# Performance work log

Measured on AMD Instinct MI355X. Metric: run time of the kernel, lower is better.

The kernel has to match this reference:

```python
import jax, jax.numpy as jnp
import numpy as np

B = 1048576
EPS = 1e-5

def _lin_params(key, din, dout):
    k1, k2 = jax.random.split(key)
    bound = 1.0 / np.sqrt(din)
    w = jax.random.uniform(k1, (din, dout), minval=-bound, maxval=bound, dtype=jnp.float32)
    b = jax.random.uniform(k2, (dout,), minval=-bound, maxval=bound, dtype=jnp.float32)
    return w, b

def setup_inputs() -> dict:
    key = jax.random.key(0)
    ks = jax.random.split(key, 10)
    x = jax.random.normal(ks[0], (B, 8), dtype=jnp.float32)
    dims = [(8, 16), (16, 16), (16, 12), (12, 8), (8, 4), (4, 4), (4, 4), (4, 1)]
    names = ['fm', 'c1', 'p1', 'c2', 'p2', 'c3', 'r', 'h']
    inp = {'x': x,
           'bn_g': jnp.ones((8,), jnp.float32),
           'bn_b': jnp.zeros((8,), jnp.float32)}
    for i, (nm, (di, do)) in enumerate(zip(names, dims)):
        w, b = _lin_params(ks[i + 1], di, do)
        inp['w_' + nm] = w
        inp['b_' + nm] = b
    return inp

def reference(x, bn_g, bn_b, w_fm, b_fm, w_c1, b_c1, w_p1, b_p1, w_c2, b_c2,
              w_p2, b_p2, w_c3, b_c3, w_r, b_r, w_h, b_h):
    # BatchNorm1d (training mode): batch statistics, biased variance
    mu = jnp.mean(x, axis=0)
    var = jnp.mean((x - mu) ** 2, axis=0)
    h = (x - mu) * jax.lax.rsqrt(var + EPS) * bn_g + bn_b
    h = jnp.tanh(h @ w_fm + b_fm)   # [B,16] feature_map
    h = jnp.tanh(h @ w_c1 + b_c1)   # [B,16] conv1
    h = jnp.tanh(h @ w_p1 + b_p1)   # [B,12] pool1
    h = jnp.tanh(h @ w_c2 + b_c2)   # [B,8]  conv2
    h = jnp.tanh(h @ w_p2 + b_p2)   # [B,4]  pool2
    h = jnp.tanh(h @ w_c3 + b_c3)   # [B,4]  conv3
    res = jax.nn.relu(h @ w_r + b_r)  # [B,4] residual branch
    h = h + res
    return jax.nn.sigmoid(h @ w_h + b_h)  # [B,1]
```

## Files before the change

### kernel.cpp

```cpp
#include <hip/hip_runtime.h>
#include <stdint.h>

#define B_ROWS 1048576
#define STAT_BLOCKS 512
#define MAIN_BLOCKS 2048

typedef __fp16 h2 __attribute__((ext_vector_type(2)));

#define PART_OFF 16
#define WPK_OFF 8208
#define BIA_OFF 8578
#define W_FM 0
#define W_C1 64
#define W_P1 192
#define W_C2 288
#define W_P2 336
#define W_C3 352
#define W_R  360
#define W_H  368
#define B_FM 0
#define B_C1 16
#define B_P1 32
#define B_C2 44
#define B_P2 52
#define B_C3 56
#define B_R  60
#define B_H  64

__device__ __forceinline__ float exp_tanh(float x) {
    float e = __builtin_amdgcn_exp2f(x * 2.8853900817779268f);
    return 1.0f - 2.0f * __builtin_amdgcn_rcpf(e + 1.0f);
}

__device__ __forceinline__ float fast_sigmoid(float x) {
    float e = __builtin_amdgcn_exp2f(x * -1.4426950408889634f);
    return __builtin_amdgcn_rcpf(1.0f + e);
}

template<int DIN, int DOUT>
__device__ void pack_layer(const float* __restrict__ w, const float* __restrict__ b,
                           uint32_t* __restrict__ wdst, float* __restrict__ bdst) {
    for (int idx = threadIdx.x; idx < DOUT * (DIN / 2); idx += blockDim.x) {
        int j = idx / (DIN / 2), i2 = idx % (DIN / 2);
        h2 h;
        h.x = (__fp16)w[(2 * i2) * DOUT + j];
        h.y = (__fp16)w[(2 * i2 + 1) * DOUT + j];
        wdst[j * (DIN / 2) + i2] = __builtin_bit_cast(uint32_t, h);
    }
    for (int j = threadIdx.x; j < DOUT; j += blockDim.x) bdst[j] = b[j];
}

__global__ __launch_bounds__(256) void bn_stats(
    const float* __restrict__ x, float* __restrict__ ws,
    const float* __restrict__ w_fm, const float* __restrict__ b_fm,
    const float* __restrict__ w_c1, const float* __restrict__ b_c1,
    const float* __restrict__ w_p1, const float* __restrict__ b_p1,
    const float* __restrict__ w_c2, const float* __restrict__ b_c2,
    const float* __restrict__ w_p2, const float* __restrict__ b_p2,
    const float* __restrict__ w_c3, const float* __restrict__ b_c3,
    const float* __restrict__ w_r,  const float* __restrict__ b_r,
    const float* __restrict__ w_h,  const float* __restrict__ b_h)
{
    const int tid = blockIdx.x * 256 + threadIdx.x;
    float s[8], q[8];
#pragma unroll
    for (int c = 0; c < 8; ++c) { s[c] = 0.f; q[c] = 0.f; }
    const float4* x4 = (const float4*)x;
#pragma unroll
    for (int k = 0; k < 8; ++k) {
        int r = tid + k * 131072;
        float4 a = x4[2 * r];
        float4 b = x4[2 * r + 1];
        s[0] += a.x; s[1] += a.y; s[2] += a.z; s[3] += a.w;
        s[4] += b.x; s[5] += b.y; s[6] += b.z; s[7] += b.w;
        q[0] += a.x * a.x; q[1] += a.y * a.y; q[2] += a.z * a.z; q[3] += a.w * a.w;
        q[4] += b.x * b.x; q[5] += b.y * b.y; q[6] += b.z * b.z; q[7] += b.w * b.w;
    }
#pragma unroll
    for (int off = 32; off > 0; off >>= 1) {
#pragma unroll
        for (int c = 0; c < 8; ++c) {
            s[c] += __shfl_down(s[c], off);
            q[c] += __shfl_down(q[c], off);
        }
    }
    __shared__ float red[4][16];
    const int lane = threadIdx.x & 63;
    const int wave = threadIdx.x >> 6;
    if (lane == 0) {
#pragma unroll
        for (int c = 0; c < 8; ++c) { red[wave][c] = s[c]; red[wave][8 + c] = q[c]; }
    }
    __syncthreads();
    if (threadIdx.x < 16) {
        float acc = red[0][threadIdx.x] + red[1][threadIdx.x] +
                    red[2][threadIdx.x] + red[3][threadIdx.x];
        ws[PART_OFF + blockIdx.x * 16 + threadIdx.x] = acc;
    }
    if (blockIdx.x == 0) {
        uint32_t* wpk = (uint32_t*)(ws + WPK_OFF);
        float*    bpk = ws + BIA_OFF;
        pack_layer<8, 16>(w_fm, b_fm, wpk + W_FM, bpk + B_FM);
        pack_layer<16,16>(w_c1, b_c1, wpk + W_C1, bpk + B_C1);
        pack_layer<16,12>(w_p1, b_p1, wpk + W_P1, bpk + B_P1);
        pack_layer<12, 8>(w_c2, b_c2, wpk + W_C2, bpk + B_C2);
        pack_layer<8,  4>(w_p2, b_p2, wpk + W_P2, bpk + B_P2);
        pack_layer<4,  4>(w_c3, b_c3, wpk + W_C3, bpk + B_C3);
        pack_layer<4,  4>(w_r,  b_r,  wpk + W_R,  bpk + B_R);
        pack_layer<4,  1>(w_h,  b_h,  wpk + W_H,  bpk + B_H);
    }
}

__device__ __forceinline__ float lut_tanh(float x, const float* __restrict__ lut) {
    float t = fmaf(x, 1024.0f, 4096.0f);
    t = __builtin_amdgcn_fmed3f(t, 0.0f, 8191.0f);
    return lut[(int)t];
}

template<int DIN, int DOUT>
__device__ __forceinline__ void layer_dot(const h2* __restrict__ apkA, const h2* __restrict__ apkB,
                                          float* __restrict__ outA, float* __restrict__ outB,
                                          const uint32_t* __restrict__ wpk,
                                          const float* __restrict__ bias) {
#pragma unroll
    for (int j = 0; j < DOUT; ++j) {
        float accA = bias[j];
        float accB = accA;
#pragma unroll
        for (int i2 = 0; i2 < DIN / 2; ++i2) {
            h2 w = __builtin_bit_cast(h2, wpk[j * (DIN / 2) + i2]);
            accA = __builtin_amdgcn_fdot2(apkA[i2], w, accA, false);
            accB = __builtin_amdgcn_fdot2(apkB[i2], w, accB, false);
        }
        outA[j] = accA;
        outB[j] = accB;
    }
}

template<int N>
__device__ __forceinline__ void tanh_pack(const float* __restrict__ inA, const float* __restrict__ inB,
                                          h2* __restrict__ pkA, h2* __restrict__ pkB,
                                          const float* __restrict__ lut) {
#pragma unroll
    for (int k = 0; k < N / 2; ++k) {
        float a0 = lut_tanh(inA[2 * k], lut);
        float a1 = lut_tanh(inA[2 * k + 1], lut);
        float b0 = lut_tanh(inB[2 * k], lut);
        float b1 = lut_tanh(inB[2 * k + 1], lut);
        pkA[k] = __builtin_amdgcn_cvt_pkrtz(a0, a1);
        pkB[k] = __builtin_amdgcn_cvt_pkrtz(b0, b1);
    }
}

__global__ __launch_bounds__(256) void qcnn_main(
    const float* __restrict__ x,
    const float* __restrict__ bn_g, const float* __restrict__ bn_b,
    const float* __restrict__ ws, float* __restrict__ out)
{
    const int tid = blockIdx.x * 256 + threadIdx.x;
    const int r0 = tid, r1 = tid + (B_ROWS / 2);
    const float4* x4 = (const float4*)x;
    float4 xa0 = x4[2 * r0], xa1 = x4[2 * r0 + 1];
    float4 xb0 = x4[2 * r1], xb1 = x4[2 * r1 + 1];

    __shared__ float lut[8192];
    __shared__ float accs[16][17];
    __shared__ float scs[8], shs[8];

    {
        const float h = 0.0009765625f;
#pragma unroll
        for (int k = 0; k < 32; ++k) {
            int i = threadIdx.x + k * 256;
            float xc = fmaf((float)i + 0.5f, h, -4.0f);
            lut[i] = exp_tanh(xc);
        }
    }
    {
        const int f = threadIdx.x & 15;
        const int chunk = threadIdx.x >> 4;
        const float* p = ws + PART_OFF + (chunk * 32) * 16 + f;
        float a = 0.f;
#pragma unroll 8
        for (int b = 0; b < 32; ++b) a += p[b * 16];
        accs[chunk][f] = a;
    }
    __syncthreads();
    if (threadIdx.x < 16) {
        float t = 0.f;
#pragma unroll
        for (int c = 0; c < 16; ++c) t += accs[c][threadIdx.x];
        accs[0][threadIdx.x] = t;
    }
    __syncthreads();
    if (threadIdx.x < 8) {
        const float invB = 1.0f / (float)B_ROWS;
        int c = threadIdx.x;
        float mu  = accs[0][c] * invB;
        float var = fmaf(-mu, mu, accs[0][8 + c] * invB);
        float s   = bn_g[c] * rsqrtf(var + 1e-5f);
        scs[c] = s;
        shs[c] = fmaf(-mu, s, bn_b[c]);
    }
    __syncthreads();

    float sc[8], sh[8];
#pragma unroll
    for (int c = 0; c < 8; ++c) { sc[c] = scs[c]; sh[c] = shs[c]; }

    const uint32_t* wpk = (const uint32_t*)(ws + WPK_OFF);
    const float*    bpk = ws + BIA_OFF;

    float nA[8], nB[8];
    nA[0] = fmaf(xa0.x, sc[0], sh[0]); nA[1] = fmaf(xa0.y, sc[1], sh[1]);
    nA[2] = fmaf(xa0.z, sc[2], sh[2]); nA[3] = fmaf(xa0.w, sc[3], sh[3]);
    nA[4] = fmaf(xa1.x, sc[4], sh[4]); nA[5] = fmaf(xa1.y, sc[5], sh[5]);
    nA[6] = fmaf(xa1.z, sc[6], sh[6]); nA[7] = fmaf(xa1.w, sc[7], sh[7]);
    nB[0] = fmaf(xb0.x, sc[0], sh[0]); nB[1] = fmaf(xb0.y, sc[1], sh[1]);
    nB[2] = fmaf(xb0.z, sc[2], sh[2]); nB[3] = fmaf(xb0.w, sc[3], sh[3]);
    nB[4] = fmaf(xb1.x, sc[4], sh[4]); nB[5] = fmaf(xb1.y, sc[5], sh[5]);
    nB[6] = fmaf(xb1.z, sc[6], sh[6]); nB[7] = fmaf(xb1.w, sc[7], sh[7]);
    h2 a8[4], b8[4];
#pragma unroll
    for (int k = 0; k < 4; ++k) {
        a8[k] = __builtin_amdgcn_cvt_pkrtz(nA[2 * k], nA[2 * k + 1]);
        b8[k] = __builtin_amdgcn_cvt_pkrtz(nB[2 * k], nB[2 * k + 1]);
    }

    float oA[16], oB[16]; h2 pA[8], pB[8];
    layer_dot<8, 16>(a8, b8, oA, oB, wpk + W_FM, bpk + B_FM);
    tanh_pack<16>(oA, oB, pA, pB, lut);
    float o2A[16], o2B[16]; h2 p2A[8], p2B[8];
    layer_dot<16,16>(pA, pB, o2A, o2B, wpk + W_C1, bpk + B_C1);
    tanh_pack<16>(o2A, o2B, p2A, p2B, lut);
    float o3A[12], o3B[12]; h2 p3A[6], p3B[6];
    layer_dot<16,12>(p2A, p2B, o3A, o3B, wpk + W_P1, bpk + B_P1);
    tanh_pack<12>(o3A, o3B, p3A, p3B, lut);
    float o4A[8], o4B[8]; h2 p4A[4], p4B[4];
    layer_dot<12, 8>(p3A, p3B, o4A, o4B, wpk + W_C2, bpk + B_C2);
    tanh_pack<8>(o4A, o4B, p4A, p4B, lut);
    float o5A[4], o5B[4]; h2 p5A[2], p5B[2];
    layer_dot<8,  4>(p4A, p4B, o5A, o5B, wpk + W_P2, bpk + B_P2);
    tanh_pack<4>(o5A, o5B, p5A, p5B, lut);
    float c4A[4], c4B[4];
    layer_dot<4,  4>(p5A, p5B, c4A, c4B, wpk + W_C3, bpk + B_C3);
#pragma unroll
    for (int j = 0; j < 4; ++j) {
        c4A[j] = lut_tanh(c4A[j], lut);
        c4B[j] = lut_tanh(c4B[j], lut);
    }
    h2 pcA[2], pcB[2];
    pcA[0] = __builtin_amdgcn_cvt_pkrtz(c4A[0], c4A[1]);
    pcA[1] = __builtin_amdgcn_cvt_pkrtz(c4A[2], c4A[3]);
    pcB[0] = __builtin_amdgcn_cvt_pkrtz(c4B[0], c4B[1]);
    pcB[1] = __builtin_amdgcn_cvt_pkrtz(c4B[2], c4B[3]);
    float r4A[4], r4B[4];
    layer_dot<4,  4>(pcA, pcB, r4A, r4B, wpk + W_R, bpk + B_R);
#pragma unroll
    for (int j = 0; j < 4; ++j) {
        c4A[j] += fmaxf(r4A[j], 0.f);
        c4B[j] += fmaxf(r4B[j], 0.f);
    }
    h2 phA[2], phB[2];
    phA[0] = __builtin_amdgcn_cvt_pkrtz(c4A[0], c4A[1]);
    phA[1] = __builtin_amdgcn_cvt_pkrtz(c4A[2], c4A[3]);
    phB[0] = __builtin_amdgcn_cvt_pkrtz(c4B[0], c4B[1]);
    phB[1] = __builtin_amdgcn_cvt_pkrtz(c4B[2], c4B[3]);
    float ohA[1], ohB[1];
    layer_dot<4,  1>(phA, phB, ohA, ohB, wpk + W_H, bpk + B_H);
    out[r0] = fast_sigmoid(ohA[0]);
    out[r1] = fast_sigmoid(ohB[0]);
}

extern "C" void kernel_launch(void* const* d_in, const int* in_sizes, int n_in,
                              void* d_out, int out_size, void* d_ws, size_t ws_size,
                              hipStream_t stream) {
    const float* x    = (const float*)d_in[0];
    const float* bn_g = (const float*)d_in[1];
    const float* bn_b = (const float*)d_in[2];
    const float* w_fm = (const float*)d_in[3];
    const float* b_fm = (const float*)d_in[4];
    const float* w_c1 = (const float*)d_in[5];
    const float* b_c1 = (const float*)d_in[6];
    const float* w_p1 = (const float*)d_in[7];
    const float* b_p1 = (const float*)d_in[8];
    const float* w_c2 = (const float*)d_in[9];
    const float* b_c2 = (const float*)d_in[10];
    const float* w_p2 = (const float*)d_in[11];
    const float* b_p2 = (const float*)d_in[12];
    const float* w_c3 = (const float*)d_in[13];
    const float* b_c3 = (const float*)d_in[14];
    const float* w_r  = (const float*)d_in[15];
    const float* b_r  = (const float*)d_in[16];
    const float* w_h  = (const float*)d_in[17];
    const float* b_h  = (const float*)d_in[18];
    float* out = (float*)d_out;
    float* ws  = (float*)d_ws;

    bn_stats<<<STAT_BLOCKS, 256, 0, stream>>>(
        x, ws, w_fm, b_fm, w_c1, b_c1, w_p1, b_p1, w_c2, b_c2,
        w_p2, b_p2, w_c3, b_c3, w_r, b_r, w_h, b_h);
    qcnn_main<<<MAIN_BLOCKS, 256, 0, stream>>>(x, bn_g, bn_b, ws, out);
}
```

Measured before the change: 142.0 us.

## Split BN finalize into own kernel, use fp16 tanh LUT, process rows sequentially

The batch-statistics finalize step moves out of every main block into a separate single-block kernel that writes scale and shift into the workspace. The tanh lookup table shrinks from fp32 to fp16, halving its LDS footprint and letting packed fp16 activations be built directly from the table entries. Each thread now runs its two rows one after the other instead of interleaved, and launch bounds request 6 blocks per CU. Together these aim to cut register and LDS pressure and per-block setup to raise occupancy, at the cost of an extra kernel launch and less ILP per thread.

```diff
diff --git a/kernel.cpp b/kernel.cpp
--- a/kernel.cpp
+++ b/kernel.cpp
@@ -111,51 +111,128 @@
     }
 }
 
-__device__ __forceinline__ float lut_tanh(float x, const float* __restrict__ lut) {
+__global__ __launch_bounds__(256) void bn_finalize(
+    const float* __restrict__ bn_g, const float* __restrict__ bn_b,
+    float* __restrict__ ws)
+{
+    __shared__ float accs[16][17];
+    const int f = threadIdx.x & 15;
+    const int chunk = threadIdx.x >> 4;
+    const float* p = ws + PART_OFF + (chunk * 32) * 16 + f;
+    float a = 0.f;
+#pragma unroll 8
+    for (int b = 0; b < 32; ++b) a += p[b * 16];
+    accs[chunk][f] = a;
+    __syncthreads();
+    if (threadIdx.x < 16) {
+        float t = 0.f;
+#pragma unroll
+        for (int c = 0; c < 16; ++c) t += accs[c][threadIdx.x];
+        accs[0][threadIdx.x] = t;
+    }
+    __syncthreads();
+    if (threadIdx.x < 8) {
+        const float invB = 1.0f / (float)B_ROWS;
+        int c = threadIdx.x;
+        float mu  = accs[0][c] * invB;
+        float var = fmaf(-mu, mu, accs[0][8 + c] * invB);
+        float sv  = bn_g[c] * rsqrtf(var + 1e-5f);
+        ws[c]     = sv;
+        ws[8 + c] = fmaf(-mu, sv, bn_b[c]);
+    }
+}
+
+__device__ __forceinline__ uint32_t lut_idx(float x) {
     float t = fmaf(x, 1024.0f, 4096.0f);
     t = __builtin_amdgcn_fmed3f(t, 0.0f, 8191.0f);
-    return lut[(int)t];
+    return (uint32_t)t;
 }
 
 template<int DIN, int DOUT>
-__device__ __forceinline__ void layer_dot(const h2* __restrict__ apkA, const h2* __restrict__ apkB,
-                                          float* __restrict__ outA, float* __restrict__ outB,
-                                          const uint32_t* __restrict__ wpk,
-                                          const float* __restrict__ bias) {
+__device__ __forceinline__ void layer_dot1(const h2* __restrict__ apk,
+                                           float* __restrict__ o,
+                                           const uint32_t* __restrict__ wpk,
+                                           const float* __restrict__ bias) {
 #pragma unroll
     for (int j = 0; j < DOUT; ++j) {
-        float accA = bias[j];
-        float accB = accA;
+        float acc = bias[j];
 #pragma unroll
         for (int i2 = 0; i2 < DIN / 2; ++i2) {
             h2 w = __builtin_bit_cast(h2, wpk[j * (DIN / 2) + i2]);
-            accA = __builtin_amdgcn_fdot2(apkA[i2], w, accA, false);
-            accB = __builtin_amdgcn_fdot2(apkB[i2], w, accB, false);
+            acc = __builtin_amdgcn_fdot2(apk[i2], w, acc, false);
         }
-        outA[j] = accA;
-        outB[j] = accB;
+        o[j] = acc;
     }
 }
 
 template<int N>
-__device__ __forceinline__ void tanh_pack(const float* __restrict__ inA, const float* __restrict__ inB,
-                                          h2* __restrict__ pkA, h2* __restrict__ pkB,
-                                          const float* __restrict__ lut) {
+__device__ __forceinline__ void tanh_pack1(const float* __restrict__ in,
+                                           h2* __restrict__ pk,
+                                           const uint16_t* __restrict__ lut16) {
 #pragma unroll
     for (int k = 0; k < N / 2; ++k) {
-        float a0 = lut_tanh(inA[2 * k], lut);
-        float a1 = lut_tanh(inA[2 * k + 1], lut);
-        float b0 = lut_tanh(inB[2 * k], lut);
-        float b1 = lut_tanh(inB[2 * k + 1], lut);
-        pkA[k] = __builtin_amdgcn_cvt_pkrtz(a0, a1);
-        pkB[k] = __builtin_amdgcn_cvt_pkrtz(b0, b1);
-    }
-}
-
-__global__ __launch_bounds__(256) void qcnn_main(
-    const float* __restrict__ x,
-    const float* __restrict__ bn_g, const float* __restrict__ bn_b,
-    const float* __restrict__ ws, float* __restrict__ out)
+        uint32_t v0 = lut16[lut_idx(in[2 * k])];
+        uint32_t v1 = lut16[lut_idx(in[2 * k + 1])];
+        pk[k] = __builtin_bit_cast(h2, v0 | (v1 << 16));
+    }
+}
+
+__device__ __forceinline__ float row_forward(float4 x0, float4 x1,
+        const float* __restrict__ sc, const float* __restrict__ sh,
+        const uint32_t* __restrict__ wpk, const float* __restrict__ bpk,
+        const uint16_t* __restrict__ lut16) {
+    float n[8];
+    n[0] = fmaf(x0.x, sc[0], sh[0]); n[1] = fmaf(x0.y, sc[1], sh[1]);
+    n[2] = fmaf(x0.z, sc[2], sh[2]); n[3] = fmaf(x0.w, sc[3], sh[3]);
+    n[4] = fmaf(x1.x, sc[4], sh[4]); n[5] = fmaf(x1.y, sc[5], sh[5]);
+    n[6] = fmaf(x1.z, sc[6], sh[6]); n[7] = fmaf(x1.w, sc[7], sh[7]);
+    h2 a[4];
+#pragma unroll
+    for (int k = 0; k < 4; ++k)
+        a[k] = __builtin_amdgcn_cvt_pkrtz(n[2 * k], n[2 * k + 1]);
+
+    float o1[16]; h2 p1[8];
+    layer_dot1<8, 16>(a, o1, wpk + W_FM, bpk + B_FM);
+    tanh_pack1<16>(o1, p1, lut16);
+    float o2[16]; h2 p2[8];
+    layer_dot1<16,16>(p1, o2, wpk + W_C1, bpk + B_C1);
+    tanh_pack1<16>(o2, p2, lut16);
+    float o3[12]; h2 p3[6];
+    layer_dot1<16,12>(p2, o3, wpk + W_P1, bpk + B_P1);
+    tanh_pack1<12>(o3, p3, lut16);
+    float o4[8]; h2 p4[4];
+    layer_dot1<12, 8>(p3, o4, wpk + W_C2, bpk + B_C2);
+    tanh_pack1<8>(o4, p4, lut16);
+    float o5[4]; h2 p5[2];
+    layer_dot1<8,  4>(p4, o5, wpk + W_P2, bpk + B_P2);
+    tanh_pack1<4>(o5, p5, lut16);
+    float c4[4];
+    layer_dot1<4,  4>(p5, c4, wpk + W_C3, bpk + B_C3);
+
+    uint32_t u[4]; float f[4];
+#pragma unroll
+    for (int j = 0; j < 4; ++j) {
+        u[j] = lut16[lut_idx(c4[j])];
+        f[j] = (float)__builtin_bit_cast(__fp16, (uint16_t)u[j]);
+    }
+    h2 pc[2];
+    pc[0] = __builtin_bit_cast(h2, u[0] | (u[1] << 16));
+    pc[1] = __builtin_bit_cast(h2, u[2] | (u[3] << 16));
+    float r4[4];
+    layer_dot1<4,  4>(pc, r4, wpk + W_R, bpk + B_R);
+#pragma unroll
+    for (int j = 0; j < 4; ++j) f[j] += fmaxf(r4[j], 0.f);
+    h2 ph[2];
+    ph[0] = __builtin_amdgcn_cvt_pkrtz(f[0], f[1]);
+    ph[1] = __builtin_amdgcn_cvt_pkrtz(f[2], f[3]);
+    float oh[1];
+    layer_dot1<4,  1>(ph, oh, wpk + W_H, bpk + B_H);
+    return fast_sigmoid(oh[0]);
+}
+
+__global__ __launch_bounds__(256, 6) void qcnn_main(
+    const float* __restrict__ x, const float* __restrict__ ws,
+    float* __restrict__ out)
 {
     const int tid = blockIdx.x * 256 + threadIdx.x;
     const int r0 = tid, r1 = tid + (B_ROWS / 2);
@@ -163,113 +240,31 @@
     float4 xa0 = x4[2 * r0], xa1 = x4[2 * r0 + 1];
     float4 xb0 = x4[2 * r1], xb1 = x4[2 * r1 + 1];
 
-    __shared__ float lut[8192];
-    __shared__ float accs[16][17];
-    __shared__ float scs[8], shs[8];
-
+    __shared__ uint16_t lut16[8192];
     {
         const float h = 0.0009765625f;
-#pragma unroll
-        for (int k = 0; k < 32; ++k) {
-            int i = threadIdx.x + k * 256;
-            float xc = fmaf((float)i + 0.5f, h, -4.0f);
-            lut[i] = exp_tanh(xc);
+        uint32_t* l32 = (uint32_t*)lut16;
+#pragma unroll
+        for (int k = 0; k < 16; ++k) {
+            int i2 = threadIdx.x + k * 256;
+            float c0 = fmaf((float)(2 * i2) + 0.5f, h, -4.0f);
+            float c1 = fmaf((float)(2 * i2 + 1) + 0.5f, h, -4.0f);
+            __fp16 h0 = (__fp16)exp_tanh(c0);
+            __fp16 h1 = (__fp16)exp_tanh(c1);
+            l32[i2] = (uint32_t)__builtin_bit_cast(uint16_t, h0)
+                    | ((uint32_t)__builtin_bit_cast(uint16_t, h1) << 16);
         }
     }
-    {
-        const int f = threadIdx.x & 15;
-        const int chunk = threadIdx.x >> 4;
-        const float* p = ws + PART_OFF + (chunk * 32) * 16 + f;
-        float a = 0.f;
-#pragma unroll 8
-        for (int b = 0; b < 32; ++b) a += p[b * 16];
-        accs[chunk][f] = a;
-    }
+    float sc[8], sh[8];
+#pragma unroll
+    for (int c = 0; c < 8; ++c) { sc[c] = ws[c]; sh[c] = ws[8 + c]; }
     __syncthreads();
-    if (threadIdx.x < 16) {
-        float t = 0.f;
-#pragma unroll
-        for (int c = 0; c < 16; ++c) t += accs[c][threadIdx.x];
-        accs[0][threadIdx.x] = t;
-    }
-    __syncthreads();
-    if (threadIdx.x < 8) {
-        const float invB = 1.0f / (float)B_ROWS;
-        int c = threadIdx.x;
-        float mu  = accs[0][c] * invB;
-        float var = fmaf(-mu, mu, accs[0][8 + c] * invB);
-        float s   = bn_g[c] * rsqrtf(var + 1e-5f);
-        scs[c] = s;
-        shs[c] = fmaf(-mu, s, bn_b[c]);
-    }
-    __syncthreads();
-
-    float sc[8], sh[8];
-#pragma unroll
-    for (int c = 0; c < 8; ++c) { sc[c] = scs[c]; sh[c] = shs[c]; }
 
     const uint32_t* wpk = (const uint32_t*)(ws + WPK_OFF);
     const float*    bpk = ws + BIA_OFF;
 
-    float nA[8], nB[8];
-    nA[0] = fmaf(xa0.x, sc[0], sh[0]); nA[1] = fmaf(xa0.y, sc[1], sh[1]);
-    nA[2] = fmaf(xa0.z, sc[2], sh[2]); nA[3] = fmaf(xa0.w, sc[3], sh[3]);
-    nA[4] = fmaf(xa1.x, sc[4], sh[4]); nA[5] = fmaf(xa1.y, sc[5], sh[5]);
-    nA[6] = fmaf(xa1.z, sc[6], sh[6]); nA[7] = fmaf(xa1.w, sc[7], sh[7]);
-    nB[0] = fmaf(xb0.x, sc[0], sh[0]); nB[1] = fmaf(xb0.y, sc[1], sh[1]);
-    nB[2] = fmaf(xb0.z, sc[2], sh[2]); nB[3] = fmaf(xb0.w, sc[3], sh[3]);
-    nB[4] = fmaf(xb1.x, sc[4], sh[4]); nB[5] = fmaf(xb1.y, sc[5], sh[5]);
-    nB[6] = fmaf(xb1.z, sc[6], sh[6]); nB[7] = fmaf(xb1.w, sc[7], sh[7]);
-    h2 a8[4], b8[4];
-#pragma unroll
-    for (int k = 0; k < 4; ++k) {
-        a8[k] = __builtin_amdgcn_cvt_pkrtz(nA[2 * k], nA[2 * k + 1]);
-        b8[k] = __builtin_amdgcn_cvt_pkrtz(nB[2 * k], nB[2 * k + 1]);
-    }
-
-    float oA[16], oB[16]; h2 pA[8], pB[8];
-    layer_dot<8, 16>(a8, b8, oA, oB, wpk + W_FM, bpk + B_FM);
-    tanh_pack<16>(oA, oB, pA, pB, lut);
-    float o2A[16], o2B[16]; h2 p2A[8], p2B[8];
-    layer_dot<16,16>(pA, pB, o2A, o2B, wpk + W_C1, bpk + B_C1);
-    tanh_pack<16>(o2A, o2B, p2A, p2B, lut);
-    float o3A[12], o3B[12]; h2 p3A[6], p3B[6];
-    layer_dot<16,12>(p2A, p2B, o3A, o3B, wpk + W_P1, bpk + B_P1);
-    tanh_pack<12>(o3A, o3B, p3A, p3B, lut);
-    float o4A[8], o4B[8]; h2 p4A[4], p4B[4];
-    layer_dot<12, 8>(p3A, p3B, o4A, o4B, wpk + W_C2, bpk + B_C2);
-    tanh_pack<8>(o4A, o4B, p4A, p4B, lut);
-    float o5A[4], o5B[4]; h2 p5A[2], p5B[2];
-    layer_dot<8,  4>(p4A, p4B, o5A, o5B, wpk + W_P2, bpk + B_P2);
-    tanh_pack<4>(o5A, o5B, p5A, p5B, lut);
-    float c4A[4], c4B[4];
-    layer_dot<4,  4>(p5A, p5B, c4A, c4B, wpk + W_C3, bpk + B_C3);
-#pragma unroll
-    for (int j = 0; j < 4; ++j) {
-        c4A[j] = lut_tanh(c4A[j], lut);
-        c4B[j] = lut_tanh(c4B[j], lut);
-    }
-    h2 pcA[2], pcB[2];
-    pcA[0] = __builtin_amdgcn_cvt_pkrtz(c4A[0], c4A[1]);
-    pcA[1] = __builtin_amdgcn_cvt_pkrtz(c4A[2], c4A[3]);
-    pcB[0] = __builtin_amdgcn_cvt_pkrtz(c4B[0], c4B[1]);
-    pcB[1] = __builtin_amdgcn_cvt_pkrtz(c4B[2], c4B[3]);
-    float r4A[4], r4B[4];
-    layer_dot<4,  4>(pcA, pcB, r4A, r4B, wpk + W_R, bpk + B_R);
-#pragma unroll
-    for (int j = 0; j < 4; ++j) {
-        c4A[j] += fmaxf(r4A[j], 0.f);
-        c4B[j] += fmaxf(r4B[j], 0.f);
-    }
-    h2 phA[2], phB[2];
-    phA[0] = __builtin_amdgcn_cvt_pkrtz(c4A[0], c4A[1]);
-    phA[1] = __builtin_amdgcn_cvt_pkrtz(c4A[2], c4A[3]);
-    phB[0] = __builtin_amdgcn_cvt_pkrtz(c4B[0], c4B[1]);
-    phB[1] = __builtin_amdgcn_cvt_pkrtz(c4B[2], c4B[3]);
-    float ohA[1], ohB[1];
-    layer_dot<4,  1>(phA, phB, ohA, ohB, wpk + W_H, bpk + B_H);
-    out[r0] = fast_sigmoid(ohA[0]);
-    out[r1] = fast_sigmoid(ohB[0]);
+    out[r0] = row_forward(xa0, xa1, sc, sh, wpk, bpk, lut16);
+    out[r1] = row_forward(xb0, xb1, sc, sh, wpk, bpk, lut16);
 }
 
 extern "C" void kernel_launch(void* const* d_in, const int* in_sizes, int n_in,
@@ -300,5 +295,6 @@
     bn_stats<<<STAT_BLOCKS, 256, 0, stream>>>(
         x, ws, w_fm, b_fm, w_c1, b_c1, w_p1, b_p1, w_c2, b_c2,
         w_p2, b_p2, w_c3, b_c3, w_r, b_r, w_h, b_h);
-    qcnn_main<<<MAIN_BLOCKS, 256, 0, stream>>>(x, bn_g, bn_b, ws, out);
-}
+    bn_finalize<<<1, 256, 0, stream>>>(bn_g, bn_b, ws);
+    qcnn_main<<<MAIN_BLOCKS, 256, 0, stream>>>(x, ws, out);
+}
```

Result: no change. 141.0 us (-0.7%).

## Replace shared-memory tanh LUT with direct exp-based tanh and adjacent-row pairing

Applied to the files above, without the earlier changes.

Removes the 32KB per-block shared tanh lookup table and its per-block construction, computing tanh directly through exp_tanh in registers. This removes the LUT build cost in every block and the LDS footprint that limited occupancy, and launch bounds now request 4 blocks per SIMD. Each thread now processes two adjacent rows, so x loads are contiguous 64-byte reads and the outputs go out as one float2 store. The tradeoff is more ALU work per activation, since each tanh now needs an exp and a divide instead of a table load, plus possible register pressure from the occupancy hint.

```diff
diff --git a/kernel.cpp b/kernel.cpp
--- a/kernel.cpp
+++ b/kernel.cpp
@@ -111,12 +111,6 @@
     }
 }
 
-__device__ __forceinline__ float lut_tanh(float x, const float* __restrict__ lut) {
-    float t = fmaf(x, 1024.0f, 4096.0f);
-    t = __builtin_amdgcn_fmed3f(t, 0.0f, 8191.0f);
-    return lut[(int)t];
-}
-
 template<int DIN, int DOUT>
 __device__ __forceinline__ void layer_dot(const h2* __restrict__ apkA, const h2* __restrict__ apkB,
                                           float* __restrict__ outA, float* __restrict__ outB,
@@ -139,43 +133,31 @@
 
 template<int N>
 __device__ __forceinline__ void tanh_pack(const float* __restrict__ inA, const float* __restrict__ inB,
-                                          h2* __restrict__ pkA, h2* __restrict__ pkB,
-                                          const float* __restrict__ lut) {
+                                          h2* __restrict__ pkA, h2* __restrict__ pkB) {
 #pragma unroll
     for (int k = 0; k < N / 2; ++k) {
-        float a0 = lut_tanh(inA[2 * k], lut);
-        float a1 = lut_tanh(inA[2 * k + 1], lut);
-        float b0 = lut_tanh(inB[2 * k], lut);
-        float b1 = lut_tanh(inB[2 * k + 1], lut);
+        float a0 = exp_tanh(inA[2 * k]);
+        float a1 = exp_tanh(inA[2 * k + 1]);
+        float b0 = exp_tanh(inB[2 * k]);
+        float b1 = exp_tanh(inB[2 * k + 1]);
         pkA[k] = __builtin_amdgcn_cvt_pkrtz(a0, a1);
         pkB[k] = __builtin_amdgcn_cvt_pkrtz(b0, b1);
     }
 }
 
-__global__ __launch_bounds__(256) void qcnn_main(
+__global__ __launch_bounds__(256, 4) void qcnn_main(
     const float* __restrict__ x,
     const float* __restrict__ bn_g, const float* __restrict__ bn_b,
     const float* __restrict__ ws, float* __restrict__ out)
 {
     const int tid = blockIdx.x * 256 + threadIdx.x;
-    const int r0 = tid, r1 = tid + (B_ROWS / 2);
     const float4* x4 = (const float4*)x;
-    float4 xa0 = x4[2 * r0], xa1 = x4[2 * r0 + 1];
-    float4 xb0 = x4[2 * r1], xb1 = x4[2 * r1 + 1];
-
-    __shared__ float lut[8192];
+    float4 xa0 = x4[4 * tid],     xa1 = x4[4 * tid + 1];
+    float4 xb0 = x4[4 * tid + 2], xb1 = x4[4 * tid + 3];
+
     __shared__ float accs[16][17];
     __shared__ float scs[8], shs[8];
 
-    {
-        const float h = 0.0009765625f;
-#pragma unroll
-        for (int k = 0; k < 32; ++k) {
-            int i = threadIdx.x + k * 256;
-            float xc = fmaf((float)i + 0.5f, h, -4.0f);
-            lut[i] = exp_tanh(xc);
-        }
-    }
     {
         const int f = threadIdx.x & 15;
         const int chunk = threadIdx.x >> 4;
@@ -198,9 +180,9 @@
         int c = threadIdx.x;
         float mu  = accs[0][c] * invB;
         float var = fmaf(-mu, mu, accs[0][8 + c] * invB);
-        float s   = bn_g[c] * rsqrtf(var + 1e-5f);
-        scs[c] = s;
-        shs[c] = fmaf(-mu, s, bn_b[c]);
+        float sv  = bn_g[c] * rsqrtf(var + 1e-5f);
+        scs[c] = sv;
+        shs[c] = fmaf(-mu, sv, bn_b[c]);
     }
     __syncthreads();
 
@@ -229,25 +211,25 @@
 
     float oA[16], oB[16]; h2 pA[8], pB[8];
     layer_dot<8, 16>(a8, b8, oA, oB, wpk + W_FM, bpk + B_FM);
-    tanh_pack<16>(oA, oB, pA, pB, lut);
+    tanh_pack<16>(oA, oB, pA, pB);
     float o2A[16], o2B[16]; h2 p2A[8], p2B[8];
     layer_dot<16,16>(pA, pB, o2A, o2B, wpk + W_C1, bpk + B_C1);
-    tanh_pack<16>(o2A, o2B, p2A, p2B, lut);
+    tanh_pack<16>(o2A, o2B, p2A, p2B);
     float o3A[12], o3B[12]; h2 p3A[6], p3B[6];
     layer_dot<16,12>(p2A, p2B, o3A, o3B, wpk + W_P1, bpk + B_P1);
-    tanh_pack<12>(o3A, o3B, p3A, p3B, lut);
+    tanh_pack<12>(o3A, o3B, p3A, p3B);
     float o4A[8], o4B[8]; h2 p4A[4], p4B[4];
     layer_dot<12, 8>(p3A, p3B, o4A, o4B, wpk + W_C2, bpk + B_C2);
-    tanh_pack<8>(o4A, o4B, p4A, p4B, lut);
+    tanh_pack<8>(o4A, o4B, p4A, p4B);
     float o5A[4], o5B[4]; h2 p5A[2], p5B[2];
     layer_dot<8,  4>(p4A, p4B, o5A, o5B, wpk + W_P2, bpk + B_P2);
-    tanh_pack<4>(o5A, o5B, p5A, p5B, lut);
+    tanh_pack<4>(o5A, o5B, p5A, p5B);
     float c4A[4], c4B[4];
     layer_dot<4,  4>(p5A, p5B, c4A, c4B, wpk + W_C3, bpk + B_C3);
 #pragma unroll
     for (int j = 0; j < 4; ++j) {
-        c4A[j] = lut_tanh(c4A[j], lut);
-        c4B[j] = lut_tanh(c4B[j], lut);
+        c4A[j] = exp_tanh(c4A[j]);
+        c4B[j] = exp_tanh(c4B[j]);
     }
     h2 pcA[2], pcB[2];
     pcA[0] = __builtin_amdgcn_cvt_pkrtz(c4A[0], c4A[1]);
@@ -268,8 +250,10 @@
     phB[1] = __builtin_amdgcn_cvt_pkrtz(c4B[2], c4B[3]);
     float ohA[1], ohB[1];
     layer_dot<4,  1>(phA, phB, ohA, ohB, wpk + W_H, bpk + B_H);
-    out[r0] = fast_sigmoid(ohA[0]);
-    out[r1] = fast_sigmoid(ohB[0]);
+    float2 o2;
+    o2.x = fast_sigmoid(ohA[0]);
+    o2.y = fast_sigmoid(ohB[0]);
+    ((float2*)out)[tid] = o2;
 }
 
 extern "C" void kernel_launch(void* const* d_in, const int* in_sizes, int n_in,
```

Measured after the change: 143.5 us. About the same (+1.0%).
